# Kernel optimization log

Hardware: AMD Instinct MI355X
Metric: run time of the kernel (lower is better)

## Reference

```python
import jax, jax.numpy as jnp
import numpy as np

EMBED_DIM = 1024
NUM_HEADS = 16
HEAD_DIM = EMBED_DIM // NUM_HEADS
B, L = 32, 2049
LN_EPS = 1e-5


def setup_inputs() -> dict:
    key = jax.random.key(0)
    ks = jax.random.split(key, 11)
    s = 1.0 / np.sqrt(EMBED_DIM)
    x = jax.random.normal(ks[0], (B, L, EMBED_DIM), dtype=jnp.float32)
    Wq = jax.random.normal(ks[1], (EMBED_DIM, EMBED_DIM), dtype=jnp.float32) * s
    bq = jnp.zeros((EMBED_DIM,), dtype=jnp.float32)
    Wk = jax.random.normal(ks[2], (EMBED_DIM, EMBED_DIM), dtype=jnp.float32) * s
    bk = jnp.zeros((EMBED_DIM,), dtype=jnp.float32)
    Wv = jax.random.normal(ks[3], (EMBED_DIM, EMBED_DIM), dtype=jnp.float32) * s
    bv = jnp.zeros((EMBED_DIM,), dtype=jnp.float32)
    Wo = jax.random.normal(ks[4], (EMBED_DIM, EMBED_DIM), dtype=jnp.float32) * s
    bo = jnp.zeros((EMBED_DIM,), dtype=jnp.float32)
    ln_g = jnp.ones((EMBED_DIM,), dtype=jnp.float32)
    ln_b = jnp.zeros((EMBED_DIM,), dtype=jnp.float32)
    return {"x": x, "Wq": Wq, "bq": bq, "Wk": Wk, "bk": bk, "Wv": Wv,
            "bv": bv, "Wo": Wo, "bo": bo, "ln_g": ln_g, "ln_b": ln_b}


def reference(x, Wq, bq, Wk, bk, Wv, bv, Wo, bo, ln_g, ln_b):
    # x: [B, L, D]; CLS token attends to the other L-1 tokens (dropout = eval/identity)
    cls_tok = x[:, 0, :]              # [B, D]
    others = x[:, 1:, :]              # [B, L-1, D]
    q = cls_tok @ Wq.T + bq           # [B, D]
    k = others @ Wk.T + bk            # [B, L-1, D]
    v = others @ Wv.T + bv            # [B, L-1, D]
    q = q.reshape(q.shape[0], NUM_HEADS, HEAD_DIM)                       # [B, H, d]
    k = k.reshape(k.shape[0], k.shape[1], NUM_HEADS, HEAD_DIM)           # [B, S, H, d]
    v = v.reshape(v.shape[0], v.shape[1], NUM_HEADS, HEAD_DIM)           # [B, S, H, d]
    scores = jnp.einsum('bhd,bshd->bhs', q, k) / np.sqrt(HEAD_DIM)       # [B, H, S]
    w = jax.nn.softmax(scores, axis=-1)
    attn = jnp.einsum('bhs,bshd->bhd', w, v)                             # [B, H, d]
    attn = attn.reshape(attn.shape[0], NUM_HEADS * HEAD_DIM)             # [B, D]
    out = attn @ Wo.T + bo
    y = out + cls_tok
    mu = jnp.mean(y, axis=-1, keepdims=True)
    var = jnp.var(y, axis=-1, keepdims=True)
    return (y - mu) / jnp.sqrt(var + LN_EPS) * ln_g + ln_b               # [B, D]
```

## Files before the change

### kernel.cpp

```cpp
#include <hip/hip_runtime.h>
#include <math.h>

#define B_ 32
#define L_ 2049
#define E_ 1024
#define H_ 16
#define NT_ 8
#define STILE 256
#define EC 32

#define OFF_Q     0
#define OFF_T     (OFF_Q + B_*E_)
#define OFF_QBK   (OFF_T + B_*H_*E_)
#define OFF_M     (OFF_QBK + B_*H_)
#define OFF_L     (OFF_M + B_*NT_*H_)
#define OFF_U     (OFF_L + B_*NT_*H_)
#define OFF_ATTN  (OFF_U + B_*H_*E_)
#define OFF_Y     (OFF_ATTN + B_*E_)
#define OFF_UP    (OFF_Y + B_*E_)

__global__ __launch_bounds__(256) void k_gemm32(const float* __restrict__ A, long long As, int mode,
                                                const float* __restrict__ W,
                                                const float* __restrict__ bias,
                                                const float* __restrict__ resid, long long Rs,
                                                float* __restrict__ C) {
    __shared__ float wls[2 * 1056];
    const int j0 = blockIdx.x * 2, tid = threadIdx.x;
    #pragma unroll
    for (int k = 0; k < 2; ++k) {
        int idx4 = k * 256 + tid;
        int row = idx4 >> 8, c4 = idx4 & 255;
        float4 v = *(const float4*)(W + (size_t)(j0 + row) * E_ + 4 * c4);
        *(float4*)&wls[row * 1056 + 4 * c4 + ((c4 >> 5) << 2)] = v;
    }
    __syncthreads();
    const int bb = tid >> 3, kseg = tid & 7;
    const long long kbase = (mode == 1) ? (long long)(j0 >> 6) * E_ : 0;
    const float* arow = A + (size_t)bb * As + kbase + kseg * 128;
    float a0 = 0.f, a1 = 0.f;
    #pragma unroll 4
    for (int i = 0; i < 32; ++i) {
        float4 av = *(const float4*)(arow + 4 * i);
        const float* wb = &wls[kseg * 132 + 4 * i];
        float4 w0 = *(const float4*)(wb);
        float4 w1 = *(const float4*)(wb + 1056);
        a0 += av.x * w0.x + av.y * w0.y + av.z * w0.z + av.w * w0.w;
        a1 += av.x * w1.x + av.y * w1.y + av.z * w1.z + av.w * w1.w;
    }
    #pragma unroll
    for (int off = 4; off; off >>= 1) {
        a0 += __shfl_down(a0, off, 8);
        a1 += __shfl_down(a1, off, 8);
    }
    if (kseg == 0) {
        float r0 = a0 + bias[j0], r1 = a1 + bias[j0 + 1];
        if (resid) {
            r0 += resid[(size_t)bb * Rs + j0];
            r1 += resid[(size_t)bb * Rs + j0 + 1];
        }
        C[(size_t)bb * E_ + j0] = r0;
        C[(size_t)bb * E_ + j0 + 1] = r1;
    }
}

__global__ __launch_bounds__(256) void k_tproj(const float* __restrict__ Wk,
                                               const float* __restrict__ bk,
                                               float* __restrict__ ws) {
    __shared__ float qs[64 * 33];
    __shared__ float wls[64 * 68];
    const int h = blockIdx.x, e0 = blockIdx.y * 64, tid = threadIdx.x;
    const float* q = ws + OFF_Q;
    #pragma unroll
    for (int k = 0; k < 8; ++k) {
        int idx = k * 256 + tid;
        int b = idx >> 6, d = idx & 63;
        qs[d * 33 + b] = q[(size_t)b * E_ + 64 * h + d];
    }
    #pragma unroll
    for (int k = 0; k < 4; ++k) {
        int idx4 = k * 256 + tid;
        int d = idx4 >> 4, c4 = idx4 & 15;
        float4 v = *(const float4*)(Wk + (size_t)(64 * h + d) * E_ + e0 + 4 * c4);
        *(float4*)&wls[d * 68 + 4 * c4] = v;
    }
    __syncthreads();
    const int el = tid & 63, bq8 = tid >> 6;
    float acc[8];
    #pragma unroll
    for (int i = 0; i < 8; ++i) acc[i] = 0.f;
    for (int d = 0; d < 64; ++d) {
        float wv = wls[d * 68 + el];
        #pragma unroll
        for (int i = 0; i < 8; ++i) acc[i] += qs[d * 33 + (bq8 * 8 + i)] * wv;
    }
    float* t = ws + OFF_T;
    #pragma unroll
    for (int i = 0; i < 8; ++i)
        t[((size_t)(bq8 * 8 + i) * H_ + h) * E_ + e0 + el] = acc[i] * 0.125f;
    if (e0 == 0 && tid < 32) {
        float s = 0.f;
        for (int d = 0; d < 64; ++d) s += qs[d * 33 + tid] * bk[64 * h + d];
        ws[OFF_QBK + tid * H_ + h] = s * 0.125f;
    }
}

__global__ __launch_bounds__(512) void k_attn_core(const float* __restrict__ x,
                                                   float* __restrict__ ws) {
    const int tile = blockIdx.x, b = blockIdx.y, tid = threadIdx.x;
    const int s0 = tile * STILE;
    const float* tmat = ws + OFF_T + (size_t)b * H_ * E_;
    const float* xb = x + (size_t)(b * L_ + 1 + s0) * E_;

    __shared__ float xs[18432];
    __shared__ float ts[1152];
    __shared__ float wl[STILE * 20];
    __shared__ float red[512];
    __shared__ float msh[16];

    const int lane = tid & 63;
    const int w = tid >> 6;

    float acc[16][4];
    #pragma unroll
    for (int hh = 0; hh < 16; ++hh)
        #pragma unroll
        for (int si = 0; si < 4; ++si) acc[hh][si] = 0.f;

    float4 xr[4];
    float tr;
    const int th = tid >> 5, te = tid & 31;
    {
        #pragma unroll
        for (int k = 0; k < 4; ++k) {
            int idx4 = k * 512 + tid, s = idx4 >> 3, e4 = idx4 & 7;
            xr[k] = *(const float4*)(xb + (size_t)s * E_ + 4 * e4);
        }
        tr = tmat[th * E_ + te];
        #pragma unroll
        for (int k = 0; k < 4; ++k) {
            int idx4 = k * 512 + tid, s = idx4 >> 3, e4 = idx4 & 7;
            *(float4*)&xs[s * 36 + 4 * e4] = xr[k];
        }
        ts[th * 36 + te] = tr;
    }
    for (int c = 0; c < 32; ++c) {
        __syncthreads();
        if (c + 1 < 32) {
            int ec = (c + 1) * EC;
            #pragma unroll
            for (int k = 0; k < 4; ++k) {
                int idx4 = k * 512 + tid, s = idx4 >> 3, e4 = idx4 & 7;
                xr[k] = *(const float4*)(xb + (size_t)s * E_ + ec + 4 * e4);
            }
            tr = tmat[th * E_ + ec + te];
        }
        const int bx = (c & 1) * 9216, bt = (c & 1) * 576;
        float4 xv[4];
        #pragma unroll
        for (int si = 0; si < 4; ++si)
            xv[si] = *(const float4*)&xs[bx + (lane + 64 * si) * 36 + 4 * w];
        #pragma unroll
        for (int hb = 0; hb < 4; ++hb) {
            float4 t0 = *(const float4*)&ts[bt + (4 * hb + 0) * 36 + 4 * w];
            float4 t1 = *(const float4*)&ts[bt + (4 * hb + 1) * 36 + 4 * w];
            float4 t2 = *(const float4*)&ts[bt + (4 * hb + 2) * 36 + 4 * w];
            float4 t3 = *(const float4*)&ts[bt + (4 * hb + 3) * 36 + 4 * w];
            #pragma unroll
            for (int si = 0; si < 4; ++si) {
                acc[4 * hb + 0][si] += t0.x * xv[si].x + t0.y * xv[si].y + t0.z * xv[si].z + t0.w * xv[si].w;
                acc[4 * hb + 1][si] += t1.x * xv[si].x + t1.y * xv[si].y + t1.z * xv[si].z + t1.w * xv[si].w;
                acc[4 * hb + 2][si] += t2.x * xv[si].x + t2.y * xv[si].y + t2.z * xv[si].z + t2.w * xv[si].w;
                acc[4 * hb + 3][si] += t3.x * xv[si].x + t3.y * xv[si].y + t3.z * xv[si].z + t3.w * xv[si].w;
            }
        }
        if (c + 1 < 32) {
            const int nx = ((c + 1) & 1) * 9216, nt = ((c + 1) & 1) * 576;
            #pragma unroll
            for (int k = 0; k < 4; ++k) {
                int idx4 = k * 512 + tid, s = idx4 >> 3, e4 = idx4 & 7;
                *(float4*)&xs[nx + s * 36 + 4 * e4] = xr[k];
            }
            ts[nt + th * 36 + te] = tr;
        }
    }
    __syncthreads();
    if (w >= 4) {
        float* pl = xs + (w - 4) * 4352;
        #pragma unroll
        for (int hh = 0; hh < 16; ++hh)
            #pragma unroll
            for (int si = 0; si < 4; ++si) pl[(lane + 64 * si) * 17 + hh] = acc[hh][si];
    }
    __syncthreads();
    if (w < 4) {
        const float* pl = xs + w * 4352;
        #pragma unroll
        for (int hh = 0; hh < 16; ++hh)
            #pragma unroll
            for (int si = 0; si < 4; ++si) acc[hh][si] += pl[(lane + 64 * si) * 17 + hh];
    }
    __syncthreads();
    if (w == 2 || w == 3) {
        float* pl = xs + (w - 2) * 4352;
        #pragma unroll
        for (int hh = 0; hh < 16; ++hh)
            #pragma unroll
            for (int si = 0; si < 4; ++si) pl[(lane + 64 * si) * 17 + hh] = acc[hh][si];
    }
    __syncthreads();
    if (w < 2) {
        const float* pl = xs + w * 4352;
        #pragma unroll
        for (int hh = 0; hh < 16; ++hh)
            #pragma unroll
            for (int si = 0; si < 4; ++si) acc[hh][si] += pl[(lane + 64 * si) * 17 + hh];
    }
    __syncthreads();
    if (w == 1) {
        float* pl = xs;
        #pragma unroll
        for (int hh = 0; hh < 16; ++hh)
            #pragma unroll
            for (int si = 0; si < 4; ++si) pl[(lane + 64 * si) * 17 + hh] = acc[hh][si];
    }
    __syncthreads();
    if (w == 0) {
        const float* pl = xs;
        const float* qbkp = ws + OFF_QBK + b * H_;
        #pragma unroll
        for (int hh = 0; hh < 16; ++hh) {
            float qb = qbkp[hh];
            #pragma unroll
            for (int si = 0; si < 4; ++si)
                wl[(lane + 64 * si) * 20 + hh] = acc[hh][si] + pl[(lane + 64 * si) * 17 + hh] + qb;
        }
    }
    __syncthreads();

    const int sh = tid & 15, seg = tid >> 4;
    {
        float m = -1e30f;
        #pragma unroll
        for (int i = 0; i < 8; ++i) m = fmaxf(m, wl[(seg * 8 + i) * 20 + sh]);
        red[seg * 16 + sh] = m;
    }
    __syncthreads();
    if (tid < 16) {
        float mm = -1e30f;
        for (int g = 0; g < 32; ++g) mm = fmaxf(mm, red[g * 16 + tid]);
        msh[tid] = mm;
    }
    __syncthreads();
    {
        float M = msh[sh];
        float ps = 0.f;
        #pragma unroll
        for (int i = 0; i < 8; ++i) {
            int idx = (seg * 8 + i) * 20 + sh;
            float v = __expf(wl[idx] - M);
            wl[idx] = v;
            ps += v;
        }
        __syncthreads();
        red[seg * 16 + sh] = ps;
    }
    __syncthreads();
    if (tid < 16) {
        float ss = 0.f;
        for (int g = 0; g < 32; ++g) ss += red[g * 16 + tid];
        ws[OFF_M + (b * NT_ + tile) * H_ + tid] = msh[tid];
        ws[OFF_L + (b * NT_ + tile) * H_ + tid] = ss;
    }

    float acc2[4][16];
    #pragma unroll
    for (int i = 0; i < 4; ++i)
        #pragma unroll
        for (int j = 0; j < 16; ++j) acc2[i][j] = 0.f;
    const int hq = 4 * (w & 3), rbase = 4 * (w >> 2);

    float4 xr2[4];
    #pragma unroll
    for (int k = 0; k < 4; ++k) {
        int idx4 = k * 512 + tid, r = idx4 >> 8, c4 = idx4 & 255;
        xr2[k] = *(const float4*)(xb + (size_t)r * E_ + 4 * c4);
    }
    __syncthreads();
    #pragma unroll
    for (int k = 0; k < 4; ++k) {
        int idx4 = k * 512 + tid, r = idx4 >> 8, c4 = idx4 & 255;
        *(float4*)&xs[r * 1028 + 4 * c4] = xr2[k];
    }
    for (int c = 0; c < 32; ++c) {
        __syncthreads();
        if (c + 1 < 32) {
            int sc = (c + 1) * 8;
            #pragma unroll
            for (int k = 0; k < 4; ++k) {
                int idx4 = k * 512 + tid, r = idx4 >> 8, c4 = idx4 & 255;
                xr2[k] = *(const float4*)(xb + (size_t)(sc + r) * E_ + 4 * c4);
            }
        }
        const int base = (c & 1) * 8224;
        #pragma unroll
        for (int rl = 0; rl < 4; ++rl) {
            const int r = rbase + rl;
            float4 wv = *(const float4*)&wl[(c * 8 + r) * 20 + hq];
            #pragma unroll
            for (int ej = 0; ej < 4; ++ej) {
                float4 xv = *(const float4*)&xs[base + r * 1028 + 4 * lane + 256 * ej];
                acc2[0][4 * ej + 0] += wv.x * xv.x; acc2[0][4 * ej + 1] += wv.x * xv.y;
                acc2[0][4 * ej + 2] += wv.x * xv.z; acc2[0][4 * ej + 3] += wv.x * xv.w;
                acc2[1][4 * ej + 0] += wv.y * xv.x; acc2[1][4 * ej + 1] += wv.y * xv.y;
                acc2[1][4 * ej + 2] += wv.y * xv.z; acc2[1][4 * ej + 3] += wv.y * xv.w;
                acc2[2][4 * ej + 0] += wv.z * xv.x; acc2[2][4 * ej + 1] += wv.z * xv.y;
                acc2[2][4 * ej + 2] += wv.z * xv.z; acc2[2][4 * ej + 3] += wv.z * xv.w;
                acc2[3][4 * ej + 0] += wv.w * xv.x; acc2[3][4 * ej + 1] += wv.w * xv.y;
                acc2[3][4 * ej + 2] += wv.w * xv.z; acc2[3][4 * ej + 3] += wv.w * xv.w;
            }
        }
        if (c + 1 < 32) {
            const int nb = ((c + 1) & 1) * 8224;
            #pragma unroll
            for (int k = 0; k < 4; ++k) {
                int idx4 = k * 512 + tid, r = idx4 >> 8, c4 = idx4 & 255;
                *(float4*)&xs[nb + r * 1028 + 4 * c4] = xr2[k];
            }
        }
    }
    __syncthreads();
    if (w >= 4) {
        const int qd = w & 3;
        #pragma unroll
        for (int hl = 0; hl < 4; ++hl)
            #pragma unroll
            for (int ej = 0; ej < 4; ++ej) {
                float4 o = make_float4(acc2[hl][4 * ej + 0], acc2[hl][4 * ej + 1],
                                       acc2[hl][4 * ej + 2], acc2[hl][4 * ej + 3]);
                *(float4*)&xs[qd * 4352 + hl * 1024 + 4 * lane + 256 * ej] = o;
            }
    }
    __syncthreads();
    if (w < 4) {
        float* up = ws + OFF_UP + (size_t)((b * NT_ + tile) * H_) * E_;
        #pragma unroll
        for (int hl = 0; hl < 4; ++hl)
            #pragma unroll
            for (int ej = 0; ej < 4; ++ej) {
                float4 pv = *(const float4*)&xs[w * 4352 + hl * 1024 + 4 * lane + 256 * ej];
                float4 o = make_float4(acc2[hl][4 * ej + 0] + pv.x, acc2[hl][4 * ej + 1] + pv.y,
                                       acc2[hl][4 * ej + 2] + pv.z, acc2[hl][4 * ej + 3] + pv.w);
                *(float4*)(up + (size_t)(hq + hl) * E_ + 4 * lane + 256 * ej) = o;
            }
    }
}

__global__ __launch_bounds__(256) void k_combine(float* __restrict__ ws) {
    const int b = blockIdx.x, h = blockIdx.y, tid = threadIdx.x;
    float m[NT_], l[NT_], f[NT_];
    float M = -1e30f;
    #pragma unroll
    for (int tg = 0; tg < NT_; ++tg) {
        m[tg] = ws[OFF_M + (b * NT_ + tg) * H_ + h];
        l[tg] = ws[OFF_L + (b * NT_ + tg) * H_ + h];
        M = fmaxf(M, m[tg]);
    }
    float Ls = 0.f;
    #pragma unroll
    for (int tg = 0; tg < NT_; ++tg) {
        f[tg] = __expf(m[tg] - M);
        Ls += f[tg] * l[tg];
    }
    const float inv = 1.f / Ls;
    float4 a = make_float4(0.f, 0.f, 0.f, 0.f);
    #pragma unroll
    for (int tg = 0; tg < NT_; ++tg) {
        float4 v = *(const float4*)(ws + OFF_UP + (size_t)((b * NT_ + tg) * H_ + h) * E_ + 4 * tid);
        a.x += f[tg] * v.x; a.y += f[tg] * v.y; a.z += f[tg] * v.z; a.w += f[tg] * v.w;
    }
    a.x *= inv; a.y *= inv; a.z *= inv; a.w *= inv;
    *(float4*)(ws + OFF_U + (size_t)(b * H_ + h) * E_ + 4 * tid) = a;
}

__global__ __launch_bounds__(256) void k_ln(const float* __restrict__ ws,
                                            const float* __restrict__ g,
                                            const float* __restrict__ be,
                                            float* __restrict__ out) {
    const int b = blockIdx.x, tid = threadIdx.x;
    const float* y = ws + OFF_Y + (size_t)b * E_;
    float4 v = *(const float4*)(y + 4 * tid);
    float s = v.x + v.y + v.z + v.w;
    float s2 = v.x * v.x + v.y * v.y + v.z * v.z + v.w * v.w;
    for (int o = 32; o; o >>= 1) {
        s += __shfl_down(s, o, 64);
        s2 += __shfl_down(s2, o, 64);
    }
    __shared__ float rs[4], rs2[4];
    int ww = tid >> 6;
    if ((tid & 63) == 0) { rs[ww] = s; rs2[ww] = s2; }
    __syncthreads();
    float S = rs[0] + rs[1] + rs[2] + rs[3];
    float S2 = rs2[0] + rs2[1] + rs2[2] + rs2[3];
    float mean = S * (1.f / 1024.f);
    float var = S2 * (1.f / 1024.f) - mean * mean;
    float r = rsqrtf(var + 1e-5f);
    float4 gv = *(const float4*)(g + 4 * tid);
    float4 bb2 = *(const float4*)(be + 4 * tid);
    float4 o;
    o.x = (v.x - mean) * r * gv.x + bb2.x;
    o.y = (v.y - mean) * r * gv.y + bb2.y;
    o.z = (v.z - mean) * r * gv.z + bb2.z;
    o.w = (v.w - mean) * r * gv.w + bb2.w;
    *(float4*)(out + (size_t)b * E_ + 4 * tid) = o;
}

extern "C" void kernel_launch(void* const* d_in, const int* in_sizes, int n_in,
                              void* d_out, int out_size, void* d_ws, size_t ws_size,
                              hipStream_t stream) {
    const float* x  = (const float*)d_in[0];
    const float* Wq = (const float*)d_in[1];
    const float* bq = (const float*)d_in[2];
    const float* Wk = (const float*)d_in[3];
    const float* bk = (const float*)d_in[4];
    const float* Wv = (const float*)d_in[5];
    const float* bv = (const float*)d_in[6];
    const float* Wo = (const float*)d_in[7];
    const float* bo = (const float*)d_in[8];
    const float* g  = (const float*)d_in[9];
    const float* be = (const float*)d_in[10];
    float* ws = (float*)d_ws;
    float* out = (float*)d_out;

    k_gemm32<<<512, 256, 0, stream>>>(x, (long long)L_ * E_, 0, Wq, bq, nullptr, 0, ws + OFF_Q);
    k_tproj<<<dim3(16, 16), 256, 0, stream>>>(Wk, bk, ws);
    k_attn_core<<<dim3(NT_, B_), 512, 0, stream>>>(x, ws);
    k_combine<<<dim3(B_, H_), 256, 0, stream>>>(ws);
    k_gemm32<<<512, 256, 0, stream>>>(ws + OFF_U, (long long)H_ * E_, 1, Wv, bv, nullptr, 0, ws + OFF_ATTN);
    k_gemm32<<<512, 256, 0, stream>>>(ws + OFF_ATTN, (long long)E_, 0, Wo, bo, x, (long long)L_ * E_, ws + OFF_Y);
    k_ln<<<B_, 256, 0, stream>>>(ws, g, be, out);
}
```

Baseline: 512.8 us.

## Split attention into smaller sequence tiles, stream x directly, store partials as bf16

The attention core now uses 128-token tiles with 256-thread blocks, doubling the grid to 16 tiles per batch for better occupancy across CUs. The score reduction switches to a warp shuffle plus a single shared-memory sum. The weighted-value pass reads x straight from global memory instead of staging it through LDS. Partial per-tile outputs are written as bf16 to halve the workspace traffic in the combine step, which costs some precision in the unnormalised partial sums.

```diff
diff --git a/kernel.cpp b/kernel.cpp
--- a/kernel.cpp
+++ b/kernel.cpp
@@ -5,9 +5,8 @@
 #define L_ 2049
 #define E_ 1024
 #define H_ 16
-#define NT_ 8
-#define STILE 256
-#define EC 32
+#define NT_ 16
+#define STILE 128
 
 #define OFF_Q     0
 #define OFF_T     (OFF_Q + B_*E_)
@@ -18,6 +17,13 @@
 #define OFF_ATTN  (OFF_U + B_*H_*E_)
 #define OFF_Y     (OFF_ATTN + B_*E_)
 #define OFF_UP    (OFF_Y + B_*E_)
+
+__device__ __forceinline__ unsigned bf16pair(float a, float b) {
+    unsigned ua = __float_as_uint(a), ub = __float_as_uint(b);
+    ua = (ua + 0x7FFFu + ((ua >> 16) & 1u)) >> 16;
+    ub = (ub + 0x7FFFu + ((ub >> 16) & 1u)) >> 16;
+    return ua | (ub << 16);
+}
 
 __global__ __launch_bounds__(256) void k_gemm32(const float* __restrict__ A, long long As, int mode,
                                                 const float* __restrict__ W,
@@ -104,135 +110,119 @@
     }
 }
 
-__global__ __launch_bounds__(512) void k_attn_core(const float* __restrict__ x,
+__global__ __launch_bounds__(256) void k_attn_core(const float* __restrict__ x,
                                                    float* __restrict__ ws) {
     const int tile = blockIdx.x, b = blockIdx.y, tid = threadIdx.x;
-    const int s0 = tile * STILE;
     const float* tmat = ws + OFF_T + (size_t)b * H_ * E_;
-    const float* xb = x + (size_t)(b * L_ + 1 + s0) * E_;
-
-    __shared__ float xs[18432];
+    const float* xb = x + (size_t)(b * L_ + 1 + tile * STILE) * E_;
+
+    __shared__ float xs[9216];
     __shared__ float ts[1152];
-    __shared__ float wl[STILE * 20];
-    __shared__ float red[512];
+    __shared__ float wl[128 * 20];
+    __shared__ float red[256];
     __shared__ float msh[16];
 
-    const int lane = tid & 63;
-    const int w = tid >> 6;
+    const int lane = tid & 63, w = tid >> 6;
+    const int sl = lane & 31, eh = lane >> 5;
+    const int qd = 2 * w + eh;
 
     float acc[16][4];
     #pragma unroll
-    for (int hh = 0; hh < 16; ++hh)
-        #pragma unroll
-        for (int si = 0; si < 4; ++si) acc[hh][si] = 0.f;
+    for (int h = 0; h < 16; ++h)
+        #pragma unroll
+        for (int si = 0; si < 4; ++si) acc[h][si] = 0.f;
 
     float4 xr[4];
-    float tr;
-    const int th = tid >> 5, te = tid & 31;
+    float tr[2];
     {
         #pragma unroll
         for (int k = 0; k < 4; ++k) {
-            int idx4 = k * 512 + tid, s = idx4 >> 3, e4 = idx4 & 7;
+            int i4 = k * 256 + tid, s = i4 >> 3, e4 = i4 & 7;
             xr[k] = *(const float4*)(xb + (size_t)s * E_ + 4 * e4);
         }
-        tr = tmat[th * E_ + te];
+        #pragma unroll
+        for (int k = 0; k < 2; ++k) {
+            int idx = k * 256 + tid, hh = idx >> 5, e = idx & 31;
+            tr[k] = tmat[hh * E_ + e];
+        }
         #pragma unroll
         for (int k = 0; k < 4; ++k) {
-            int idx4 = k * 512 + tid, s = idx4 >> 3, e4 = idx4 & 7;
+            int i4 = k * 256 + tid, s = i4 >> 3, e4 = i4 & 7;
             *(float4*)&xs[s * 36 + 4 * e4] = xr[k];
         }
-        ts[th * 36 + te] = tr;
+        #pragma unroll
+        for (int k = 0; k < 2; ++k) {
+            int idx = k * 256 + tid, hh = idx >> 5, e = idx & 31;
+            ts[hh * 36 + e] = tr[k];
+        }
     }
     for (int c = 0; c < 32; ++c) {
         __syncthreads();
         if (c + 1 < 32) {
-            int ec = (c + 1) * EC;
+            int ec = (c + 1) * 32;
             #pragma unroll
             for (int k = 0; k < 4; ++k) {
-                int idx4 = k * 512 + tid, s = idx4 >> 3, e4 = idx4 & 7;
+                int i4 = k * 256 + tid, s = i4 >> 3, e4 = i4 & 7;
                 xr[k] = *(const float4*)(xb + (size_t)s * E_ + ec + 4 * e4);
             }
-            tr = tmat[th * E_ + ec + te];
-        }
-        const int bx = (c & 1) * 9216, bt = (c & 1) * 576;
+            #pragma unroll
+            for (int k = 0; k < 2; ++k) {
+                int idx = k * 256 + tid, hh = idx >> 5, e = idx & 31;
+                tr[k] = tmat[hh * E_ + ec + e];
+            }
+        }
+        const int bx = (c & 1) * 4608, bt = (c & 1) * 576;
         float4 xv[4];
         #pragma unroll
         for (int si = 0; si < 4; ++si)
-            xv[si] = *(const float4*)&xs[bx + (lane + 64 * si) * 36 + 4 * w];
-        #pragma unroll
-        for (int hb = 0; hb < 4; ++hb) {
-            float4 t0 = *(const float4*)&ts[bt + (4 * hb + 0) * 36 + 4 * w];
-            float4 t1 = *(const float4*)&ts[bt + (4 * hb + 1) * 36 + 4 * w];
-            float4 t2 = *(const float4*)&ts[bt + (4 * hb + 2) * 36 + 4 * w];
-            float4 t3 = *(const float4*)&ts[bt + (4 * hb + 3) * 36 + 4 * w];
-            #pragma unroll
-            for (int si = 0; si < 4; ++si) {
-                acc[4 * hb + 0][si] += t0.x * xv[si].x + t0.y * xv[si].y + t0.z * xv[si].z + t0.w * xv[si].w;
-                acc[4 * hb + 1][si] += t1.x * xv[si].x + t1.y * xv[si].y + t1.z * xv[si].z + t1.w * xv[si].w;
-                acc[4 * hb + 2][si] += t2.x * xv[si].x + t2.y * xv[si].y + t2.z * xv[si].z + t2.w * xv[si].w;
-                acc[4 * hb + 3][si] += t3.x * xv[si].x + t3.y * xv[si].y + t3.z * xv[si].z + t3.w * xv[si].w;
-            }
+            xv[si] = *(const float4*)&xs[bx + (sl + 32 * si) * 36 + 4 * qd];
+        #pragma unroll
+        for (int h = 0; h < 16; ++h) {
+            float4 tf = *(const float4*)&ts[bt + h * 36 + 4 * qd];
+            #pragma unroll
+            for (int si = 0; si < 4; ++si)
+                acc[h][si] += tf.x * xv[si].x + tf.y * xv[si].y + tf.z * xv[si].z + tf.w * xv[si].w;
         }
         if (c + 1 < 32) {
-            const int nx = ((c + 1) & 1) * 9216, nt = ((c + 1) & 1) * 576;
+            const int nx = ((c + 1) & 1) * 4608, nt = ((c + 1) & 1) * 576;
             #pragma unroll
             for (int k = 0; k < 4; ++k) {
-                int idx4 = k * 512 + tid, s = idx4 >> 3, e4 = idx4 & 7;
+                int i4 = k * 256 + tid, s = i4 >> 3, e4 = i4 & 7;
                 *(float4*)&xs[nx + s * 36 + 4 * e4] = xr[k];
             }
-            ts[nt + th * 36 + te] = tr;
-        }
-    }
-    __syncthreads();
-    if (w >= 4) {
-        float* pl = xs + (w - 4) * 4352;
-        #pragma unroll
-        for (int hh = 0; hh < 16; ++hh)
-            #pragma unroll
-            for (int si = 0; si < 4; ++si) pl[(lane + 64 * si) * 17 + hh] = acc[hh][si];
-    }
-    __syncthreads();
-    if (w < 4) {
-        const float* pl = xs + w * 4352;
-        #pragma unroll
-        for (int hh = 0; hh < 16; ++hh)
-            #pragma unroll
-            for (int si = 0; si < 4; ++si) acc[hh][si] += pl[(lane + 64 * si) * 17 + hh];
-    }
-    __syncthreads();
-    if (w == 2 || w == 3) {
-        float* pl = xs + (w - 2) * 4352;
-        #pragma unroll
-        for (int hh = 0; hh < 16; ++hh)
-            #pragma unroll
-            for (int si = 0; si < 4; ++si) pl[(lane + 64 * si) * 17 + hh] = acc[hh][si];
-    }
-    __syncthreads();
-    if (w < 2) {
-        const float* pl = xs + w * 4352;
-        #pragma unroll
-        for (int hh = 0; hh < 16; ++hh)
-            #pragma unroll
-            for (int si = 0; si < 4; ++si) acc[hh][si] += pl[(lane + 64 * si) * 17 + hh];
-    }
-    __syncthreads();
-    if (w == 1) {
-        float* pl = xs;
-        #pragma unroll
-        for (int hh = 0; hh < 16; ++hh)
-            #pragma unroll
-            for (int si = 0; si < 4; ++si) pl[(lane + 64 * si) * 17 + hh] = acc[hh][si];
-    }
-    __syncthreads();
-    if (w == 0) {
-        const float* pl = xs;
-        const float* qbkp = ws + OFF_QBK + b * H_;
-        #pragma unroll
-        for (int hh = 0; hh < 16; ++hh) {
-            float qb = qbkp[hh];
-            #pragma unroll
-            for (int si = 0; si < 4; ++si)
-                wl[(lane + 64 * si) * 20 + hh] = acc[hh][si] + pl[(lane + 64 * si) * 17 + hh] + qb;
+            #pragma unroll
+            for (int k = 0; k < 2; ++k) {
+                int idx = k * 256 + tid, hh = idx >> 5, e = idx & 31;
+                ts[nt + hh * 36 + e] = tr[k];
+            }
+        }
+    }
+    __syncthreads();
+
+    #pragma unroll
+    for (int h = 0; h < 16; ++h)
+        #pragma unroll
+        for (int si = 0; si < 4; ++si)
+            acc[h][si] += __shfl_xor(acc[h][si], 32, 64);
+    {
+        float* pl = xs + w * 2176;
+        #pragma unroll
+        for (int si = 0; si < 4; ++si) {
+            int s = sl + 32 * si;
+            #pragma unroll
+            for (int hh = 0; hh < 8; ++hh)
+                pl[s * 17 + 8 * eh + hh] = acc[8 * eh + hh][si];
+        }
+    }
+    __syncthreads();
+    {
+        const float* qbk = ws + OFF_QBK + b * H_;
+        #pragma unroll
+        for (int i = 0; i < 8; ++i) {
+            int o = tid * 8 + i, s = o >> 4, h = o & 15;
+            float v = xs[s * 17 + h] + xs[2176 + s * 17 + h] +
+                      xs[4352 + s * 17 + h] + xs[6528 + s * 17 + h] + qbk[h];
+            wl[s * 20 + h] = v;
         }
     }
     __syncthreads();
@@ -247,7 +237,7 @@
     __syncthreads();
     if (tid < 16) {
         float mm = -1e30f;
-        for (int g = 0; g < 32; ++g) mm = fmaxf(mm, red[g * 16 + tid]);
+        for (int g = 0; g < 16; ++g) mm = fmaxf(mm, red[g * 16 + tid]);
         msh[tid] = mm;
     }
     __syncthreads();
@@ -267,91 +257,57 @@
     __syncthreads();
     if (tid < 16) {
         float ss = 0.f;
-        for (int g = 0; g < 32; ++g) ss += red[g * 16 + tid];
+        for (int g = 0; g < 16; ++g) ss += red[g * 16 + tid];
         ws[OFF_M + (b * NT_ + tile) * H_ + tid] = msh[tid];
         ws[OFF_L + (b * NT_ + tile) * H_ + tid] = ss;
     }
 
-    float acc2[4][16];
-    #pragma unroll
-    for (int i = 0; i < 4; ++i)
-        #pragma unroll
-        for (int j = 0; j < 16; ++j) acc2[i][j] = 0.f;
-    const int hq = 4 * (w & 3), rbase = 4 * (w >> 2);
-
-    float4 xr2[4];
-    #pragma unroll
-    for (int k = 0; k < 4; ++k) {
-        int idx4 = k * 512 + tid, r = idx4 >> 8, c4 = idx4 & 255;
-        xr2[k] = *(const float4*)(xb + (size_t)r * E_ + 4 * c4);
-    }
-    __syncthreads();
-    #pragma unroll
-    for (int k = 0; k < 4; ++k) {
-        int idx4 = k * 512 + tid, r = idx4 >> 8, c4 = idx4 & 255;
-        *(float4*)&xs[r * 1028 + 4 * c4] = xr2[k];
-    }
-    for (int c = 0; c < 32; ++c) {
-        __syncthreads();
-        if (c + 1 < 32) {
-            int sc = (c + 1) * 8;
-            #pragma unroll
-            for (int k = 0; k < 4; ++k) {
-                int idx4 = k * 512 + tid, r = idx4 >> 8, c4 = idx4 & 255;
-                xr2[k] = *(const float4*)(xb + (size_t)(sc + r) * E_ + 4 * c4);
-            }
-        }
-        const int base = (c & 1) * 8224;
-        #pragma unroll
-        for (int rl = 0; rl < 4; ++rl) {
-            const int r = rbase + rl;
-            float4 wv = *(const float4*)&wl[(c * 8 + r) * 20 + hq];
-            #pragma unroll
-            for (int ej = 0; ej < 4; ++ej) {
-                float4 xv = *(const float4*)&xs[base + r * 1028 + 4 * lane + 256 * ej];
-                acc2[0][4 * ej + 0] += wv.x * xv.x; acc2[0][4 * ej + 1] += wv.x * xv.y;
-                acc2[0][4 * ej + 2] += wv.x * xv.z; acc2[0][4 * ej + 3] += wv.x * xv.w;
-                acc2[1][4 * ej + 0] += wv.y * xv.x; acc2[1][4 * ej + 1] += wv.y * xv.y;
-                acc2[1][4 * ej + 2] += wv.y * xv.z; acc2[1][4 * ej + 3] += wv.y * xv.w;
-                acc2[2][4 * ej + 0] += wv.z * xv.x; acc2[2][4 * ej + 1] += wv.z * xv.y;
-                acc2[2][4 * ej + 2] += wv.z * xv.z; acc2[2][4 * ej + 3] += wv.z * xv.w;
-                acc2[3][4 * ej + 0] += wv.w * xv.x; acc2[3][4 * ej + 1] += wv.w * xv.y;
-                acc2[3][4 * ej + 2] += wv.w * xv.z; acc2[3][4 * ej + 3] += wv.w * xv.w;
-            }
-        }
-        if (c + 1 < 32) {
-            const int nb = ((c + 1) & 1) * 8224;
-            #pragma unroll
-            for (int k = 0; k < 4; ++k) {
-                int idx4 = k * 512 + tid, r = idx4 >> 8, c4 = idx4 & 255;
-                *(float4*)&xs[nb + r * 1028 + 4 * c4] = xr2[k];
-            }
-        }
-    }
-    __syncthreads();
-    if (w >= 4) {
-        const int qd = w & 3;
-        #pragma unroll
-        for (int hl = 0; hl < 4; ++hl)
-            #pragma unroll
-            for (int ej = 0; ej < 4; ++ej) {
-                float4 o = make_float4(acc2[hl][4 * ej + 0], acc2[hl][4 * ej + 1],
-                                       acc2[hl][4 * ej + 2], acc2[hl][4 * ej + 3]);
-                *(float4*)&xs[qd * 4352 + hl * 1024 + 4 * lane + 256 * ej] = o;
-            }
-    }
-    __syncthreads();
-    if (w < 4) {
-        float* up = ws + OFF_UP + (size_t)((b * NT_ + tile) * H_) * E_;
-        #pragma unroll
-        for (int hl = 0; hl < 4; ++hl)
-            #pragma unroll
-            for (int ej = 0; ej < 4; ++ej) {
-                float4 pv = *(const float4*)&xs[w * 4352 + hl * 1024 + 4 * lane + 256 * ej];
-                float4 o = make_float4(acc2[hl][4 * ej + 0] + pv.x, acc2[hl][4 * ej + 1] + pv.y,
-                                       acc2[hl][4 * ej + 2] + pv.z, acc2[hl][4 * ej + 3] + pv.w);
-                *(float4*)(up + (size_t)(hq + hl) * E_ + 4 * lane + 256 * ej) = o;
-            }
+    float acc2[16][4];
+    #pragma unroll
+    for (int h = 0; h < 16; ++h)
+        #pragma unroll
+        for (int j = 0; j < 4; ++j) acc2[h][j] = 0.f;
+    const float* xb2 = xb + w * 256 + 4 * lane;
+    for (int s = 0; s < STILE; s += 4) {
+        float4 xv[4];
+        #pragma unroll
+        for (int u = 0; u < 4; ++u)
+            xv[u] = *(const float4*)(xb2 + (size_t)(s + u) * E_);
+        #pragma unroll
+        for (int u = 0; u < 4; ++u) {
+            const float* wp = &wl[(s + u) * 20];
+            float4 w0 = *(const float4*)(wp);
+            float4 w1 = *(const float4*)(wp + 4);
+            float4 w2 = *(const float4*)(wp + 8);
+            float4 w3 = *(const float4*)(wp + 12);
+            acc2[0][0] += w0.x * xv[u].x; acc2[0][1] += w0.x * xv[u].y; acc2[0][2] += w0.x * xv[u].z; acc2[0][3] += w0.x * xv[u].w;
+            acc2[1][0] += w0.y * xv[u].x; acc2[1][1] += w0.y * xv[u].y; acc2[1][2] += w0.y * xv[u].z; acc2[1][3] += w0.y * xv[u].w;
+            acc2[2][0] += w0.z * xv[u].x; acc2[2][1] += w0.z * xv[u].y; acc2[2][2] += w0.z * xv[u].z; acc2[2][3] += w0.z * xv[u].w;
+            acc2[3][0] += w0.w * xv[u].x; acc2[3][1] += w0.w * xv[u].y; acc2[3][2] += w0.w * xv[u].z; acc2[3][3] += w0.w * xv[u].w;
+            acc2[4][0] += w1.x * xv[u].x; acc2[4][1] += w1.x * xv[u].y; acc2[4][2] += w1.x * xv[u].z; acc2[4][3] += w1.x * xv[u].w;
+            acc2[5][0] += w1.y * xv[u].x; acc2[5][1] += w1.y * xv[u].y; acc2[5][2] += w1.y * xv[u].z; acc2[5][3] += w1.y * xv[u].w;
+            acc2[6][0] += w1.z * xv[u].x; acc2[6][1] += w1.z * xv[u].y; acc2[6][2] += w1.z * xv[u].z; acc2[6][3] += w1.z * xv[u].w;
+            acc2[7][0] += w1.w * xv[u].x; acc2[7][1] += w1.w * xv[u].y; acc2[7][2] += w1.w * xv[u].z; acc2[7][3] += w1.w * xv[u].w;
+            acc2[8][0] += w2.x * xv[u].x; acc2[8][1] += w2.x * xv[u].y; acc2[8][2] += w2.x * xv[u].z; acc2[8][3] += w2.x * xv[u].w;
+            acc2[9][0] += w2.y * xv[u].x; acc2[9][1] += w2.y * xv[u].y; acc2[9][2] += w2.y * xv[u].z; acc2[9][3] += w2.y * xv[u].w;
+            acc2[10][0] += w2.z * xv[u].x; acc2[10][1] += w2.z * xv[u].y; acc2[10][2] += w2.z * xv[u].z; acc2[10][3] += w2.z * xv[u].w;
+            acc2[11][0] += w2.w * xv[u].x; acc2[11][1] += w2.w * xv[u].y; acc2[11][2] += w2.w * xv[u].z; acc2[11][3] += w2.w * xv[u].w;
+            acc2[12][0] += w3.x * xv[u].x; acc2[12][1] += w3.x * xv[u].y; acc2[12][2] += w3.x * xv[u].z; acc2[12][3] += w3.x * xv[u].w;
+            acc2[13][0] += w3.y * xv[u].x; acc2[13][1] += w3.y * xv[u].y; acc2[13][2] += w3.y * xv[u].z; acc2[13][3] += w3.y * xv[u].w;
+            acc2[14][0] += w3.z * xv[u].x; acc2[14][1] += w3.z * xv[u].y; acc2[14][2] += w3.z * xv[u].z; acc2[14][3] += w3.z * xv[u].w;
+            acc2[15][0] += w3.w * xv[u].x; acc2[15][1] += w3.w * xv[u].y; acc2[15][2] += w3.w * xv[u].z; acc2[15][3] += w3.w * xv[u].w;
+        }
+    }
+    {
+        unsigned short* up = (unsigned short*)(ws + OFF_UP) +
+                             (size_t)((b * NT_ + tile) * H_) * E_ + w * 256 + 4 * lane;
+        #pragma unroll
+        for (int h = 0; h < 16; ++h) {
+            uint2 p;
+            p.x = bf16pair(acc2[h][0], acc2[h][1]);
+            p.y = bf16pair(acc2[h][2], acc2[h][3]);
+            *(uint2*)(up + (size_t)h * E_) = p;
+        }
     }
 }
 
@@ -372,11 +328,16 @@
         Ls += f[tg] * l[tg];
     }
     const float inv = 1.f / Ls;
+    const unsigned short* up = (const unsigned short*)(ws + OFF_UP);
     float4 a = make_float4(0.f, 0.f, 0.f, 0.f);
     #pragma unroll
     for (int tg = 0; tg < NT_; ++tg) {
-        float4 v = *(const float4*)(ws + OFF_UP + (size_t)((b * NT_ + tg) * H_ + h) * E_ + 4 * tid);
-        a.x += f[tg] * v.x; a.y += f[tg] * v.y; a.z += f[tg] * v.z; a.w += f[tg] * v.w;
+        uint2 p = *(const uint2*)(up + (size_t)((b * NT_ + tg) * H_ + h) * E_ + 4 * tid);
+        float v0 = __uint_as_float((p.x & 0xFFFFu) << 16);
+        float v1 = __uint_as_float(p.x & 0xFFFF0000u);
+        float v2 = __uint_as_float((p.y & 0xFFFFu) << 16);
+        float v3 = __uint_as_float(p.y & 0xFFFF0000u);
+        a.x += f[tg] * v0; a.y += f[tg] * v1; a.z += f[tg] * v2; a.w += f[tg] * v3;
     }
     a.x *= inv; a.y *= inv; a.z *= inv; a.w *= inv;
     *(float4*)(ws + OFF_U + (size_t)(b * H_ + h) * E_ + 4 * tid) = a;
@@ -433,7 +394,7 @@
 
     k_gemm32<<<512, 256, 0, stream>>>(x, (long long)L_ * E_, 0, Wq, bq, nullptr, 0, ws + OFF_Q);
     k_tproj<<<dim3(16, 16), 256, 0, stream>>>(Wk, bk, ws);
-    k_attn_core<<<dim3(NT_, B_), 512, 0, stream>>>(x, ws);
+    k_attn_core<<<dim3(NT_, B_), 256, 0, stream>>>(x, ws);
     k_combine<<<dim3(B_, H_), 256, 0, stream>>>(ws);
     k_gemm32<<<512, 256, 0, stream>>>(ws + OFF_U, (long long)H_ * E_, 1, Wv, bv, nullptr, 0, ws + OFF_ATTN);
     k_gemm32<<<512, 256, 0, stream>>>(ws + OFF_ATTN, (long long)E_, 0, Wo, bo, x, (long long)L_ * E_, ws + OFF_Y);
```

After: 705.1 us. +37.5%, slower.
